# Performance work log

Hardware: AMD Instinct MI355X
Metric: run time of the kernel (lower is better)

The kernel has to match this reference:

```python
import jax, jax.numpy as jnp
import numpy as np

NUM_HEAD = 16

def setup_inputs() -> dict:
    rk = jax.random.key(0)
    k1, k2, k3, k4, k5 = jax.random.split(rk, 5)
    B, Sq, Skv, D = 4, 2048, 2048, 1024
    return {
        "query": jax.random.normal(k1, (B, Sq, D), dtype=jnp.float32),
        "key":   jax.random.normal(k2, (B, Skv, D), dtype=jnp.float32),
        "value": jax.random.normal(k3, (B, Skv, D), dtype=jnp.float32),
        "W": jax.random.normal(k4, (D, D), dtype=jnp.float32) * (D ** -0.5),
        "b": jax.random.normal(k5, (D,), dtype=jnp.float32) * 0.01,
    }

def reference(query, key, value, W, b):
    B, Sq, D = query.shape
    H = NUM_HEAD
    hd = D // H
    # chunk(num_head, -1) == split last dim into H contiguous heads
    q = query.reshape(B, Sq, H, hd)
    k = key.reshape(B, -1, H, hd)
    v = value.reshape(B, -1, H, hd)
    # scores[b,h,q,k] = (Q_h K_h^T) / sqrt(embedding_dim)  (full dim, per source)
    scores = jnp.einsum('bqhd,bkhd->bhqk', q, k) / jnp.sqrt(jnp.float32(D))
    # nn.Softmax(dim=1) on a [B, q, kv] matrix -> softmax over the QUERY axis
    attn = jax.nn.softmax(scores, axis=2)
    out = jnp.einsum('bhqk,bkhd->bqhd', attn, v).reshape(B, Sq, D)
    # final linear: x @ W^T + b
    return out @ W.T + b
```

## Files before the change

kernel.cpp:

```cpp
#include <hip/hip_runtime.h>

#define NH    16
#define HD    64
#define SQ    2048
#define SKV   2048
#define DM    1024

typedef __attribute__((ext_vector_type(8))) __bf16 bf16x8;
typedef __attribute__((ext_vector_type(4))) __bf16 bf16x4;
typedef __attribute__((ext_vector_type(4))) float  f32x4;

#define ASYNC16(gp, lp)                                                        \
    __builtin_amdgcn_global_load_lds(                                          \
        (const __attribute__((address_space(1))) void*)(gp),                   \
        (__attribute__((address_space(3))) void*)(lp), 16, 0, 0)

#if __has_builtin(__builtin_amdgcn_exp2f)
#define EXPS(x) __builtin_amdgcn_exp2f((x) * 0.04508422f)
#else
#define EXPS(x) __expf((x) * 0.03125f)
#endif

static __device__ __forceinline__ int swz(int row, int chunk) {
    return (row << 6) + (((chunk) ^ (row & 7)) << 3);
}

static __device__ __forceinline__ bf16x4 cvt4(float4 v) {
    bf16x4 r;
    r[0] = (__bf16)v.x; r[1] = (__bf16)v.y; r[2] = (__bf16)v.z; r[3] = (__bf16)v.w;
    return r;
}

__global__ void kprep_all(const float* __restrict__ q, const float* __restrict__ k,
                          const float* __restrict__ W,
                          __bf16* __restrict__ Qh, __bf16* __restrict__ Kh,
                          __bf16* __restrict__ Wb) {
    int bid = blockIdx.x;
    if (bid < 8192) {
        const float* src = (bid < 4096) ? q : k;
        __bf16* dst = (bid < 4096) ? Qh : Kh;
        size_t g = (size_t)(bid & 4095) * 256 + threadIdx.x;
        size_t o = g * 8;
        int c  = (int)(o & 63);
        int s  = (int)((o >> 6) & 2047);
        int bh = (int)(o >> 17);
        int b = bh >> 4, h = bh & 15;
        const float* p = src + ((size_t)(b * SQ + s)) * DM + h * HD + c;
        float4 v0 = *(const float4*)p;
        float4 v1 = *(const float4*)(p + 4);
        bf16x8 r;
        r[0] = (__bf16)v0.x; r[1] = (__bf16)v0.y; r[2] = (__bf16)v0.z; r[3] = (__bf16)v0.w;
        r[4] = (__bf16)v1.x; r[5] = (__bf16)v1.y; r[6] = (__bf16)v1.z; r[7] = (__bf16)v1.w;
        *(bf16x8*)(dst + o) = r;
    } else {
        int i = (bid - 8192) * 256 + threadIdx.x;
        float4 v = *(const float4*)(W + (size_t)i * 4);
        *(bf16x4*)(Wb + (size_t)i * 4) = cvt4(v);
    }
}

__global__ __launch_bounds__(256, 2) void kz(const __bf16* __restrict__ Qh,
                                             const __bf16* __restrict__ Kh,
                                             const float* __restrict__ v,
                                             __bf16* __restrict__ Vt) {
    const int bh = blockIdx.x;
    const int kb = blockIdx.y;
    const int b = bh >> 4, h = bh & 15;
    const int t = threadIdx.x;
    const int w = t >> 6, lane = t & 63;
    const int lo16 = lane & 15, quad = lane >> 4;
    const int wub = (t & 192) << 3;

    __shared__ __bf16 Ks[256 * 64];
    __shared__ __bf16 Qs[2][64 * 64];
    __shared__ float  Zs[256];

    const __bf16* kbase = Kh + ((size_t)bh * SKV + kb * 256) * HD;
    const __bf16* qbase = Qh + (size_t)bh * SQ * HD;

#pragma unroll
    for (int i = 0; i < 8; ++i) {
        int ci = i * 256 + t;
        int row = ci >> 3;
        int c = (ci & 7) ^ (row & 7);
        ASYNC16(kbase + row * 64 + c * 8, &Ks[i * 2048 + wub]);
    }
#pragma unroll
    for (int i = 0; i < 2; ++i) {
        int ci = i * 256 + t;
        int row = ci >> 3;
        int c = (ci & 7) ^ (row & 7);
        ASYNC16(qbase + row * 64 + c * 8, &Qs[0][i * 2048 + wub]);
    }
    __syncthreads();

    bf16x8 bk[4][2];
#pragma unroll
    for (int nt = 0; nt < 4; ++nt)
#pragma unroll
        for (int dh = 0; dh < 2; ++dh)
            bk[nt][dh] = *(const bf16x8*)(&Ks[swz(w * 64 + nt * 16 + lo16, dh * 4 + quad)]);

    float zacc[4] = {0.f, 0.f, 0.f, 0.f};

    for (int qt = 0; qt < 32; ++qt) {
        const int cur = qt & 1, nxt = cur ^ 1;
        if (qt < 31) {
#pragma unroll
            for (int i = 0; i < 2; ++i) {
                int ci = i * 256 + t;
                int row = ci >> 3;
                int c = (ci & 7) ^ (row & 7);
                ASYNC16(qbase + (size_t)(qt + 1) * 64 * HD + row * 64 + c * 8,
                        &Qs[nxt][i * 2048 + wub]);
            }
        }

#pragma unroll
        for (int mt = 0; mt < 4; ++mt) {
            bf16x8 aq0 = *(const bf16x8*)(&Qs[cur][swz(mt * 16 + lo16, quad)]);
            bf16x8 aq1 = *(const bf16x8*)(&Qs[cur][swz(mt * 16 + lo16, 4 + quad)]);
#pragma unroll
            for (int nt = 0; nt < 4; ++nt) {
                f32x4 acc = {0.f, 0.f, 0.f, 0.f};
                acc = __builtin_amdgcn_mfma_f32_16x16x32_bf16(aq0, bk[nt][0], acc, 0, 0, 0);
                acc = __builtin_amdgcn_mfma_f32_16x16x32_bf16(aq1, bk[nt][1], acc, 0, 0, 0);
                zacc[nt] += EXPS(acc[0]) + EXPS(acc[1]) + EXPS(acc[2]) + EXPS(acc[3]);
            }
        }
        __syncthreads();
    }

#pragma unroll
    for (int nt = 0; nt < 4; ++nt) {
        float s = zacc[nt];
        s += __shfl_xor(s, 16, 64);
        s += __shfl_xor(s, 32, 64);
        if (lane < 16) Zs[w * 64 + nt * 16 + lane] = s;
    }
    __syncthreads();

    {
        float rz = 1.0f / Zs[t];
        const float* vrow = v + ((size_t)(b * SKV) + kb * 256 + t) * DM + h * HD;
        size_t vtb = (size_t)bh * HD * SKV + kb * 256 + t;
#pragma unroll
        for (int dc = 0; dc < 4; ++dc) {
            float4 a0 = *(const float4*)(vrow + dc * 16 + 0);
            float4 a1 = *(const float4*)(vrow + dc * 16 + 4);
            float4 a2 = *(const float4*)(vrow + dc * 16 + 8);
            float4 a3 = *(const float4*)(vrow + dc * 16 + 12);
            float tmp[16] = {a0.x, a0.y, a0.z, a0.w, a1.x, a1.y, a1.z, a1.w,
                             a2.x, a2.y, a2.z, a2.w, a3.x, a3.y, a3.z, a3.w};
#pragma unroll
            for (int j = 0; j < 16; ++j)
                Vt[vtb + (size_t)(dc * 16 + j) * SKV] = (__bf16)(tmp[j] * rz);
        }
    }
}

__global__ __launch_bounds__(256, 2) void kattn(const __bf16* __restrict__ Qh,
                                                const __bf16* __restrict__ Kh,
                                                const __bf16* __restrict__ Vt,
                                                __bf16* __restrict__ O) {
    const int bh = blockIdx.x;
    const int qb = blockIdx.y;
    const int b = bh >> 4, h = bh & 15;
    const int t = threadIdx.x;
    const int w = t >> 6, lane = t & 63;
    const int lo16 = lane & 15, quad = lane >> 4;
    const int wub = (t & 192) << 3;

    __shared__ __bf16 Ks[2][64 * 64];
    __shared__ __bf16 Vts[2][64 * 64];
    __shared__ __bf16 QE[256 * 64];

    const __bf16* qgbase = Qh + ((size_t)bh * SQ + qb * 256) * HD;
    const __bf16* kgbase = Kh + (size_t)bh * SKV * HD;
    const __bf16* vtgbase = Vt + (size_t)bh * HD * SKV;

#pragma unroll
    for (int i = 0; i < 8; ++i) {
        int ci = i * 256 + t;
        int row = ci >> 3;
        int c = (ci & 7) ^ (row & 7);
        ASYNC16(qgbase + row * 64 + c * 8, &QE[i * 2048 + wub]);
    }
#pragma unroll
    for (int i = 0; i < 2; ++i) {
        int ci = i * 256 + t;
        int row = ci >> 3;
        int c = (ci & 7) ^ (row & 7);
        ASYNC16(kgbase + row * 64 + c * 8, &Ks[0][i * 2048 + wub]);
        ASYNC16(vtgbase + (size_t)row * SKV + c * 8, &Vts[0][i * 2048 + wub]);
    }
    __syncthreads();

    bf16x8 qf[4][2];
#pragma unroll
    for (int qt = 0; qt < 4; ++qt)
#pragma unroll
        for (int dh = 0; dh < 2; ++dh)
            qf[qt][dh] = *(const bf16x8*)(&QE[swz(w * 64 + qt * 16 + lo16, dh * 4 + quad)]);

    f32x4 oacc[4][4];
    f32x4 zero = {0.f, 0.f, 0.f, 0.f};
#pragma unroll
    for (int qt = 0; qt < 4; ++qt)
#pragma unroll
        for (int nt = 0; nt < 4; ++nt)
            oacc[qt][nt] = zero;

    __bf16* Ew = &QE[w * 64 * 64];

    for (int kt = 0; kt < 32; ++kt) {
        const int cur = kt & 1, nxt = cur ^ 1;
        if (kt < 31) {
#pragma unroll
            for (int i = 0; i < 2; ++i) {
                int ci = i * 256 + t;
                int row = ci >> 3;
                int c = (ci & 7) ^ (row & 7);
                ASYNC16(kgbase + (size_t)(kt + 1) * 64 * HD + row * 64 + c * 8,
                        &Ks[nxt][i * 2048 + wub]);
                ASYNC16(vtgbase + (size_t)row * SKV + (kt + 1) * 64 + c * 8,
                        &Vts[nxt][i * 2048 + wub]);
            }
        }

#pragma unroll
        for (int ktile = 0; ktile < 4; ++ktile) {
            bf16x8 ak0 = *(const bf16x8*)(&Ks[cur][swz(ktile * 16 + lo16, quad)]);
            bf16x8 ak1 = *(const bf16x8*)(&Ks[cur][swz(ktile * 16 + lo16, 4 + quad)]);
#pragma unroll
            for (int qt = 0; qt < 4; ++qt) {
                f32x4 s = zero;
                s = __builtin_amdgcn_mfma_f32_16x16x32_bf16(ak0, qf[qt][0], s, 0, 0, 0);
                s = __builtin_amdgcn_mfma_f32_16x16x32_bf16(ak1, qf[qt][1], s, 0, 0, 0);
                bf16x4 e;
                e[0] = (__bf16)EXPS(s[0]);
                e[1] = (__bf16)EXPS(s[1]);
                e[2] = (__bf16)EXPS(s[2]);
                e[3] = (__bf16)EXPS(s[3]);
                int er = qt * 16 + lo16;
                *(bf16x4*)(&Ew[(er << 6) + ((((2 * ktile + (quad >> 1))) ^ (er & 7)) << 3)
                               + (quad & 1) * 4]) = e;
            }
        }

#pragma unroll
        for (int kk2 = 0; kk2 < 2; ++kk2) {
            bf16x8 ae[4];
#pragma unroll
            for (int qt = 0; qt < 4; ++qt)
                ae[qt] = *(const bf16x8*)(&Ew[swz(qt * 16 + lo16, kk2 * 4 + quad)]);
#pragma unroll
            for (int nt = 0; nt < 4; ++nt) {
                bf16x8 bv = *(const bf16x8*)(&Vts[cur][swz(nt * 16 + lo16, kk2 * 4 + quad)]);
#pragma unroll
                for (int qt = 0; qt < 4; ++qt)
                    oacc[qt][nt] = __builtin_amdgcn_mfma_f32_16x16x32_bf16(ae[qt], bv, oacc[qt][nt], 0, 0, 0);
            }
        }
        __syncthreads();
    }

    size_t obase = ((size_t)(b * SQ) + qb * 256 + w * 64) * DM + h * HD;
#pragma unroll
    for (int qt = 0; qt < 4; ++qt)
#pragma unroll
        for (int nt = 0; nt < 4; ++nt)
#pragma unroll
            for (int r = 0; r < 4; ++r)
                O[obase + (size_t)(qt * 16 + quad * 4 + r) * DM + nt * 16 + lo16] =
                    (__bf16)oacc[qt][nt][r];
}

__global__ __launch_bounds__(256, 2) void kproj(const __bf16* __restrict__ A,
                                                const __bf16* __restrict__ Wb,
                                                const float* __restrict__ bias,
                                                float* __restrict__ out) {
    const int nb = blockIdx.x;
    const int mb = blockIdx.y;
    const int t = threadIdx.x;
    const int w = t >> 6, lane = t & 63;
    const int lo16 = lane & 15, quad = lane >> 4;
    const int wm = w & 1, wn = w >> 1;
    const int wub = (t & 192) << 3;

    __shared__ __bf16 As[2][128 * 64];
    __shared__ __bf16 Bs[2][128 * 64];

    f32x4 acc[4][4];
    f32x4 zero = {0.f, 0.f, 0.f, 0.f};
#pragma unroll
    for (int mt = 0; mt < 4; ++mt)
#pragma unroll
        for (int nt = 0; nt < 4; ++nt)
            acc[mt][nt] = zero;

    const __bf16* abase = A + (size_t)(mb * 128) * DM;
    const __bf16* wbase = Wb + (size_t)(nb * 128) * DM;

#pragma unroll
    for (int i = 0; i < 4; ++i) {
        int ci = i * 256 + t;
        int row = ci >> 3;
        int c = (ci & 7) ^ (row & 7);
        ASYNC16(abase + (size_t)row * DM + c * 8, &As[0][i * 2048 + wub]);
        ASYNC16(wbase + (size_t)row * DM + c * 8, &Bs[0][i * 2048 + wub]);
    }
    __syncthreads();

    for (int kt = 0; kt < 16; ++kt) {
        const int cur = kt & 1, nxt = cur ^ 1;
        if (kt < 15) {
#pragma unroll
            for (int i = 0; i < 4; ++i) {
                int ci = i * 256 + t;
                int row = ci >> 3;
                int c = (ci & 7) ^ (row & 7);
                ASYNC16(abase + (size_t)row * DM + (kt + 1) * 64 + c * 8, &As[nxt][i * 2048 + wub]);
                ASYNC16(wbase + (size_t)row * DM + (kt + 1) * 64 + c * 8, &Bs[nxt][i * 2048 + wub]);
            }
        }

#pragma unroll
        for (int ks = 0; ks < 2; ++ks) {
            bf16x8 av[4], bv[4];
#pragma unroll
            for (int mt = 0; mt < 4; ++mt)
                av[mt] = *(const bf16x8*)(&As[cur][swz(wm * 64 + mt * 16 + lo16, ks * 4 + quad)]);
#pragma unroll
            for (int nt = 0; nt < 4; ++nt)
                bv[nt] = *(const bf16x8*)(&Bs[cur][swz(wn * 64 + nt * 16 + lo16, ks * 4 + quad)]);
#pragma unroll
            for (int mt = 0; mt < 4; ++mt)
#pragma unroll
                for (int nt = 0; nt < 4; ++nt)
                    acc[mt][nt] = __builtin_amdgcn_mfma_f32_16x16x32_bf16(av[mt], bv[nt], acc[mt][nt], 0, 0, 0);
        }
        __syncthreads();
    }

    const int col0 = nb * 128 + wn * 64;
    const int row0 = mb * 128 + wm * 64;
#pragma unroll
    for (int nt = 0; nt < 4; ++nt) {
        float bb = bias[col0 + nt * 16 + lo16];
#pragma unroll
        for (int mt = 0; mt < 4; ++mt)
#pragma unroll
            for (int r = 0; r < 4; ++r)
                out[(size_t)(row0 + mt * 16 + quad * 4 + r) * DM + col0 + nt * 16 + lo16] =
                    acc[mt][nt][r] + bb;
    }
}

extern "C" void kernel_launch(void* const* d_in, const int* in_sizes, int n_in,
                              void* d_out, int out_size, void* d_ws, size_t ws_size,
                              hipStream_t stream) {
    const float* q    = (const float*)d_in[0];
    const float* k    = (const float*)d_in[1];
    const float* v    = (const float*)d_in[2];
    const float* W    = (const float*)d_in[3];
    const float* bias = (const float*)d_in[4];
    float* out = (float*)d_out;

    char* ws = (char*)d_ws;
    __bf16* Qh = (__bf16*)ws;
    __bf16* Kh = (__bf16*)(ws + (16u << 20));
    __bf16* Vt = (__bf16*)(ws + (32u << 20));
    __bf16* Wb = (__bf16*)(ws + (48u << 20));
    __bf16* O  = (__bf16*)(ws + (50u << 20));

    kprep_all<<<dim3(9216), 256, 0, stream>>>(q, k, W, Qh, Kh, Wb);
    kz       <<<dim3(64, 8), 256, 0, stream>>>(Qh, Kh, v, Vt);
    kattn    <<<dim3(64, 8), 256, 0, stream>>>(Qh, Kh, Vt, O);
    kproj    <<<dim3(8, 64), 256, 0, stream>>>(O, Wb, bias, out);
}
```

Measured before the change: 294.6 us.

## Use 512-thread blocks in kz and kattn with 32 rows per wave

The column-normalizer kernel and the attention kernel now launch 512 threads (8 waves) instead of 256, and each wave handles 32 rows instead of 64. Per-wave register arrays shrink and the launch bounds ask for 4 blocks per CU, aiming at higher occupancy and latency hiding on the same 512-block grid. kattn now loads its Q fragments straight from global memory instead of staging them in LDS, and s_setprio raises wave priority around the MFMA sections. The costs are more waves contending for the same K/V tiles and barriers, and per-wave E scratch buffers in LDS.

```diff
diff --git a/kernel.cpp b/kernel.cpp
--- a/kernel.cpp
+++ b/kernel.cpp
@@ -59,17 +59,23 @@
     }
 }
 
-__global__ __launch_bounds__(256, 2) void kz(const __bf16* __restrict__ Qh,
+__global__ __launch_bounds__(512, 4) void kz(const __bf16* __restrict__ Qh,
                                              const __bf16* __restrict__ Kh,
-                                             const float* __restrict__ v,
+                                             const __bf16* __restrict__ v,
+                                             __bf16* __restrict__ Vt);
+
+__global__ __launch_bounds__(512, 4) void kz(const __bf16* __restrict__ Qh,
+                                             const __bf16* __restrict__ Kh,
+                                             const __bf16* __restrict__ vv,
                                              __bf16* __restrict__ Vt) {
+    const float* v = (const float*)vv;
     const int bh = blockIdx.x;
     const int kb = blockIdx.y;
     const int b = bh >> 4, h = bh & 15;
     const int t = threadIdx.x;
     const int w = t >> 6, lane = t & 63;
     const int lo16 = lane & 15, quad = lane >> 4;
-    const int wub = (t & 192) << 3;
+    const int wub = (t & 448) << 3;
 
     __shared__ __bf16 Ks[256 * 64];
     __shared__ __bf16 Qs[2][64 * 64];
@@ -79,73 +85,72 @@
     const __bf16* qbase = Qh + (size_t)bh * SQ * HD;
 
 #pragma unroll
-    for (int i = 0; i < 8; ++i) {
-        int ci = i * 256 + t;
+    for (int i = 0; i < 4; ++i) {
+        int ci = i * 512 + t;
         int row = ci >> 3;
         int c = (ci & 7) ^ (row & 7);
-        ASYNC16(kbase + row * 64 + c * 8, &Ks[i * 2048 + wub]);
-    }
-#pragma unroll
-    for (int i = 0; i < 2; ++i) {
-        int ci = i * 256 + t;
+        ASYNC16(kbase + row * 64 + c * 8, &Ks[i * 4096 + wub]);
+    }
+    {
+        int ci = t;
         int row = ci >> 3;
         int c = (ci & 7) ^ (row & 7);
-        ASYNC16(qbase + row * 64 + c * 8, &Qs[0][i * 2048 + wub]);
+        ASYNC16(qbase + row * 64 + c * 8, &Qs[0][wub]);
     }
     __syncthreads();
 
-    bf16x8 bk[4][2];
-#pragma unroll
-    for (int nt = 0; nt < 4; ++nt)
+    bf16x8 bk[2][2];
+#pragma unroll
+    for (int nt = 0; nt < 2; ++nt)
 #pragma unroll
         for (int dh = 0; dh < 2; ++dh)
-            bk[nt][dh] = *(const bf16x8*)(&Ks[swz(w * 64 + nt * 16 + lo16, dh * 4 + quad)]);
-
-    float zacc[4] = {0.f, 0.f, 0.f, 0.f};
+            bk[nt][dh] = *(const bf16x8*)(&Ks[swz(w * 32 + nt * 16 + lo16, dh * 4 + quad)]);
+
+    float zacc[2] = {0.f, 0.f};
 
     for (int qt = 0; qt < 32; ++qt) {
         const int cur = qt & 1, nxt = cur ^ 1;
         if (qt < 31) {
-#pragma unroll
-            for (int i = 0; i < 2; ++i) {
-                int ci = i * 256 + t;
-                int row = ci >> 3;
-                int c = (ci & 7) ^ (row & 7);
-                ASYNC16(qbase + (size_t)(qt + 1) * 64 * HD + row * 64 + c * 8,
-                        &Qs[nxt][i * 2048 + wub]);
-            }
-        }
-
+            int ci = t;
+            int row = ci >> 3;
+            int c = (ci & 7) ^ (row & 7);
+            ASYNC16(qbase + (size_t)(qt + 1) * 64 * HD + row * 64 + c * 8,
+                    &Qs[nxt][wub]);
+        }
+
+        __builtin_amdgcn_s_setprio(1);
 #pragma unroll
         for (int mt = 0; mt < 4; ++mt) {
             bf16x8 aq0 = *(const bf16x8*)(&Qs[cur][swz(mt * 16 + lo16, quad)]);
             bf16x8 aq1 = *(const bf16x8*)(&Qs[cur][swz(mt * 16 + lo16, 4 + quad)]);
 #pragma unroll
-            for (int nt = 0; nt < 4; ++nt) {
+            for (int nt = 0; nt < 2; ++nt) {
                 f32x4 acc = {0.f, 0.f, 0.f, 0.f};
                 acc = __builtin_amdgcn_mfma_f32_16x16x32_bf16(aq0, bk[nt][0], acc, 0, 0, 0);
                 acc = __builtin_amdgcn_mfma_f32_16x16x32_bf16(aq1, bk[nt][1], acc, 0, 0, 0);
                 zacc[nt] += EXPS(acc[0]) + EXPS(acc[1]) + EXPS(acc[2]) + EXPS(acc[3]);
             }
         }
+        __builtin_amdgcn_s_setprio(0);
         __syncthreads();
     }
 
 #pragma unroll
-    for (int nt = 0; nt < 4; ++nt) {
+    for (int nt = 0; nt < 2; ++nt) {
         float s = zacc[nt];
         s += __shfl_xor(s, 16, 64);
         s += __shfl_xor(s, 32, 64);
-        if (lane < 16) Zs[w * 64 + nt * 16 + lane] = s;
+        if (lane < 16) Zs[w * 32 + nt * 16 + lane] = s;
     }
     __syncthreads();
 
     {
-        float rz = 1.0f / Zs[t];
-        const float* vrow = v + ((size_t)(b * SKV) + kb * 256 + t) * DM + h * HD;
-        size_t vtb = (size_t)bh * HD * SKV + kb * 256 + t;
-#pragma unroll
-        for (int dc = 0; dc < 4; ++dc) {
+        int kcol = t & 255, dh2 = t >> 8;
+        float rz = 1.0f / Zs[kcol];
+        const float* vrow = v + ((size_t)(b * SKV) + kb * 256 + kcol) * DM + h * HD + dh2 * 32;
+        size_t vtb = (size_t)bh * HD * SKV + kb * 256 + kcol;
+#pragma unroll
+        for (int dc = 0; dc < 2; ++dc) {
             float4 a0 = *(const float4*)(vrow + dc * 16 + 0);
             float4 a1 = *(const float4*)(vrow + dc * 16 + 4);
             float4 a2 = *(const float4*)(vrow + dc * 16 + 8);
@@ -154,12 +159,12 @@
                              a2.x, a2.y, a2.z, a2.w, a3.x, a3.y, a3.z, a3.w};
 #pragma unroll
             for (int j = 0; j < 16; ++j)
-                Vt[vtb + (size_t)(dc * 16 + j) * SKV] = (__bf16)(tmp[j] * rz);
-        }
-    }
-}
-
-__global__ __launch_bounds__(256, 2) void kattn(const __bf16* __restrict__ Qh,
+                Vt[vtb + (size_t)(dh2 * 32 + dc * 16 + j) * SKV] = (__bf16)(tmp[j] * rz);
+        }
+    }
+}
+
+__global__ __launch_bounds__(512, 4) void kattn(const __bf16* __restrict__ Qh,
                                                 const __bf16* __restrict__ Kh,
                                                 const __bf16* __restrict__ Vt,
                                                 __bf16* __restrict__ O) {
@@ -169,71 +174,63 @@
     const int t = threadIdx.x;
     const int w = t >> 6, lane = t & 63;
     const int lo16 = lane & 15, quad = lane >> 4;
-    const int wub = (t & 192) << 3;
+    const int wub = (t & 448) << 3;
 
     __shared__ __bf16 Ks[2][64 * 64];
     __shared__ __bf16 Vts[2][64 * 64];
-    __shared__ __bf16 QE[256 * 64];
-
-    const __bf16* qgbase = Qh + ((size_t)bh * SQ + qb * 256) * HD;
+    __shared__ __bf16 Es[8][32 * 64];
+
+    const __bf16* qgb = Qh + ((size_t)bh * SQ + qb * 256 + w * 32) * HD;
     const __bf16* kgbase = Kh + (size_t)bh * SKV * HD;
     const __bf16* vtgbase = Vt + (size_t)bh * HD * SKV;
 
-#pragma unroll
-    for (int i = 0; i < 8; ++i) {
-        int ci = i * 256 + t;
+    {
+        int ci = t;
         int row = ci >> 3;
         int c = (ci & 7) ^ (row & 7);
-        ASYNC16(qgbase + row * 64 + c * 8, &QE[i * 2048 + wub]);
-    }
-#pragma unroll
-    for (int i = 0; i < 2; ++i) {
-        int ci = i * 256 + t;
-        int row = ci >> 3;
-        int c = (ci & 7) ^ (row & 7);
-        ASYNC16(kgbase + row * 64 + c * 8, &Ks[0][i * 2048 + wub]);
-        ASYNC16(vtgbase + (size_t)row * SKV + c * 8, &Vts[0][i * 2048 + wub]);
-    }
-    __syncthreads();
-
-    bf16x8 qf[4][2];
-#pragma unroll
-    for (int qt = 0; qt < 4; ++qt)
+        ASYNC16(kgbase + row * 64 + c * 8, &Ks[0][wub]);
+        ASYNC16(vtgbase + (size_t)row * SKV + c * 8, &Vts[0][wub]);
+    }
+
+    bf16x8 qf[2][2];
+#pragma unroll
+    for (int qt = 0; qt < 2; ++qt)
 #pragma unroll
         for (int dh = 0; dh < 2; ++dh)
-            qf[qt][dh] = *(const bf16x8*)(&QE[swz(w * 64 + qt * 16 + lo16, dh * 4 + quad)]);
-
-    f32x4 oacc[4][4];
+            qf[qt][dh] = *(const bf16x8*)(qgb + (size_t)(qt * 16 + lo16) * HD
+                                          + (dh * 4 + quad) * 8);
+
+    f32x4 oacc[2][4];
     f32x4 zero = {0.f, 0.f, 0.f, 0.f};
 #pragma unroll
-    for (int qt = 0; qt < 4; ++qt)
+    for (int qt = 0; qt < 2; ++qt)
 #pragma unroll
         for (int nt = 0; nt < 4; ++nt)
             oacc[qt][nt] = zero;
 
-    __bf16* Ew = &QE[w * 64 * 64];
+    __syncthreads();
+
+    __bf16* Ew = &Es[w][0];
 
     for (int kt = 0; kt < 32; ++kt) {
         const int cur = kt & 1, nxt = cur ^ 1;
         if (kt < 31) {
-#pragma unroll
-            for (int i = 0; i < 2; ++i) {
-                int ci = i * 256 + t;
-                int row = ci >> 3;
-                int c = (ci & 7) ^ (row & 7);
-                ASYNC16(kgbase + (size_t)(kt + 1) * 64 * HD + row * 64 + c * 8,
-                        &Ks[nxt][i * 2048 + wub]);
-                ASYNC16(vtgbase + (size_t)row * SKV + (kt + 1) * 64 + c * 8,
-                        &Vts[nxt][i * 2048 + wub]);
-            }
-        }
-
+            int ci = t;
+            int row = ci >> 3;
+            int c = (ci & 7) ^ (row & 7);
+            ASYNC16(kgbase + (size_t)(kt + 1) * 64 * HD + row * 64 + c * 8,
+                    &Ks[nxt][wub]);
+            ASYNC16(vtgbase + (size_t)row * SKV + (kt + 1) * 64 + c * 8,
+                    &Vts[nxt][wub]);
+        }
+
+        __builtin_amdgcn_s_setprio(1);
 #pragma unroll
         for (int ktile = 0; ktile < 4; ++ktile) {
             bf16x8 ak0 = *(const bf16x8*)(&Ks[cur][swz(ktile * 16 + lo16, quad)]);
             bf16x8 ak1 = *(const bf16x8*)(&Ks[cur][swz(ktile * 16 + lo16, 4 + quad)]);
 #pragma unroll
-            for (int qt = 0; qt < 4; ++qt) {
+            for (int qt = 0; qt < 2; ++qt) {
                 f32x4 s = zero;
                 s = __builtin_amdgcn_mfma_f32_16x16x32_bf16(ak0, qf[qt][0], s, 0, 0, 0);
                 s = __builtin_amdgcn_mfma_f32_16x16x32_bf16(ak1, qf[qt][1], s, 0, 0, 0);
@@ -250,24 +247,25 @@
 
 #pragma unroll
         for (int kk2 = 0; kk2 < 2; ++kk2) {
-            bf16x8 ae[4];
-#pragma unroll
-            for (int qt = 0; qt < 4; ++qt)
+            bf16x8 ae[2];
+#pragma unroll
+            for (int qt = 0; qt < 2; ++qt)
                 ae[qt] = *(const bf16x8*)(&Ew[swz(qt * 16 + lo16, kk2 * 4 + quad)]);
 #pragma unroll
             for (int nt = 0; nt < 4; ++nt) {
                 bf16x8 bv = *(const bf16x8*)(&Vts[cur][swz(nt * 16 + lo16, kk2 * 4 + quad)]);
 #pragma unroll
-                for (int qt = 0; qt < 4; ++qt)
+                for (int qt = 0; qt < 2; ++qt)
                     oacc[qt][nt] = __builtin_amdgcn_mfma_f32_16x16x32_bf16(ae[qt], bv, oacc[qt][nt], 0, 0, 0);
             }
         }
+        __builtin_amdgcn_s_setprio(0);
         __syncthreads();
     }
 
-    size_t obase = ((size_t)(b * SQ) + qb * 256 + w * 64) * DM + h * HD;
-#pragma unroll
-    for (int qt = 0; qt < 4; ++qt)
+    size_t obase = ((size_t)(b * SQ) + qb * 256 + w * 32) * DM + h * HD;
+#pragma unroll
+    for (int qt = 0; qt < 2; ++qt)
 #pragma unroll
         for (int nt = 0; nt < 4; ++nt)
 #pragma unroll
@@ -375,7 +373,7 @@
     __bf16* O  = (__bf16*)(ws + (50u << 20));
 
     kprep_all<<<dim3(9216), 256, 0, stream>>>(q, k, W, Qh, Kh, Wb);
-    kz       <<<dim3(64, 8), 256, 0, stream>>>(Qh, Kh, v, Vt);
-    kattn    <<<dim3(64, 8), 256, 0, stream>>>(Qh, Kh, Vt, O);
+    kz       <<<dim3(64, 8), 512, 0, stream>>>(Qh, Kh, (const __bf16*)v, Vt);
+    kattn    <<<dim3(64, 8), 512, 0, stream>>>(Qh, Kh, Vt, O);
     kproj    <<<dim3(8, 64), 256, 0, stream>>>(O, Wb, bias, out);
 }
```

Measured after the change: 283.3 us. 3.8% less time.
